# Performance work log

Measured on AMD Instinct MI355X. Metric: run time of the kernel, lower is better.

## Reference

```python
import jax, jax.numpy as jnp
import numpy as np

EMBED = 1024
HEADS = 16
HEAD_DIM = EMBED // HEADS
EPS = 1e-8


def setup_inputs() -> dict:
    key = jax.random.key(0)
    ks = jax.random.split(key, 10)
    s = 1.0 / np.sqrt(EMBED)
    return {
        "hidden_input": jax.random.normal(ks[0], (4, 2048, EMBED), dtype=jnp.float32),
        "Wq": jax.random.uniform(ks[1], (EMBED, EMBED), jnp.float32, -s, s),
        "bq": jax.random.uniform(ks[2], (EMBED,), jnp.float32, -s, s),
        "Wk": jax.random.uniform(ks[3], (EMBED, EMBED), jnp.float32, -s, s),
        "bk": jax.random.uniform(ks[4], (EMBED,), jnp.float32, -s, s),
        "Wv": jax.random.uniform(ks[5], (EMBED, EMBED), jnp.float32, -s, s),
        "bv": jax.random.uniform(ks[6], (EMBED,), jnp.float32, -s, s),
        "Wp": jax.random.uniform(ks[7], (EMBED, EMBED), jnp.float32, -s, s),
        "bp": jax.random.uniform(ks[8], (EMBED,), jnp.float32, -s, s),
        "gamma": jnp.ones((EMBED,), jnp.float32),
        "beta": jnp.zeros((EMBED,), jnp.float32),
    }


def reference(hidden_input, Wq, bq, Wk, bk, Wv, bv, Wp, bp, gamma, beta):
    n, l, e = hidden_input.shape
    h, d = HEADS, HEAD_DIM

    def split_heads(x):  # [n, l, e] -> [n, h, l, d]
        return x.reshape(n, l, h, d).transpose(0, 2, 1, 3)

    q = split_heads(hidden_input @ Wq + bq)
    k = split_heads(hidden_input @ Wk + bk)
    v = split_heads(hidden_input @ Wv + bv)

    scores = jnp.einsum("nhqd,nhkd->nhqk", q, k) / jnp.sqrt(jnp.float32(d))
    attn = jax.nn.softmax(scores, axis=-1)
    ctx = jnp.einsum("nhqk,nhkd->nhqd", attn, v)
    ctx = ctx.transpose(0, 2, 1, 3).reshape(n, l, e)

    out = ctx @ Wp + bp
    x = out + hidden_input
    mu = jnp.mean(x, axis=-1, keepdims=True)
    var = jnp.mean(jnp.square(x - mu), axis=-1, keepdims=True)
    return (x - mu) / jnp.sqrt(var + EPS) * gamma + beta
```

## Files before the change

### kernel.cpp

```cpp
#include <hip/hip_runtime.h>

#define EMBED 1024
#define SEQ   2048
#define BATCH 4
#define HEADS 16

typedef __attribute__((ext_vector_type(8))) short short8;
typedef __attribute__((ext_vector_type(4))) float floatx4;

#define MFMA16(a, b, c) __builtin_amdgcn_mfma_f32_16x16x32_bf16((a), (b), (c), 0, 0, 0)
#define ATT_SCALE (0.125f * 1.44269504088896340736f)

static __device__ __forceinline__ unsigned short f2bf(float f) {
  union { float f; unsigned int u; } v; v.f = f;
  unsigned int u = v.u;
  u += 0x7fffu + ((u >> 16) & 1u);
  return (unsigned short)(u >> 16);
}

static __device__ __forceinline__ void async16(const unsigned short* g, unsigned short* l) {
  __builtin_amdgcn_global_load_lds(
      (const __attribute__((address_space(1))) void*)g,
      (__attribute__((address_space(3))) void*)l, 16, 0, 0);
}

__global__ __launch_bounds__(256) void k_prep(const float* __restrict__ hid,
                                              unsigned short* __restrict__ hidA,
                                              const float* __restrict__ Wq, const float* __restrict__ Wk,
                                              const float* __restrict__ Wv, const float* __restrict__ Wp,
                                              unsigned short* __restrict__ WT) {
  __shared__ unsigned short tile[64][65];
  const int bid = blockIdx.x, tid = threadIdx.x;
  if (bid < 4096) {
    int i = bid * 256 + tid;
    const float4* s = (const float4*)hid;
    float4 a = s[i * 2], b = s[i * 2 + 1];
    uint4 o;
    o.x = (unsigned)f2bf(a.x) | ((unsigned)f2bf(a.y) << 16);
    o.y = (unsigned)f2bf(a.z) | ((unsigned)f2bf(a.w) << 16);
    o.z = (unsigned)f2bf(b.x) | ((unsigned)f2bf(b.y) << 16);
    o.w = (unsigned)f2bf(b.z) | ((unsigned)f2bf(b.w) << 16);
    ((uint4*)hidA)[i] = o;
    return;
  }
  const int idx = bid - 4096;
  const int z = idx >> 8, rem = idx & 255;
  const float* src = (z == 0) ? Wq : (z == 1) ? Wk : (z == 2) ? Wv : Wp;
  unsigned short* dst = WT + (size_t)z * EMBED * EMBED;
  const int k0 = (rem & 15) * 64, n0 = (rem >> 4) * 64;
  for (int i = tid; i < 4096; i += 256) {
    int r = i >> 6, c = i & 63;
    tile[c][r] = f2bf(src[(size_t)(k0 + r) * EMBED + n0 + c]);
  }
  __syncthreads();
  for (int i = tid; i < 4096; i += 256) {
    int r = i >> 6, c = i & 63;
    dst[(size_t)(n0 + r) * EMBED + k0 + c] = tile[r][c];
  }
}

__global__ __launch_bounds__(256) void k_gemm_qkv(const unsigned short* __restrict__ A,
                                                  const unsigned short* __restrict__ BT,
                                                  const float* __restrict__ bq,
                                                  const float* __restrict__ bk,
                                                  const float* __restrict__ bv,
                                                  unsigned short* __restrict__ C) {
  __shared__ unsigned short Als[128 * 64];
  __shared__ unsigned short Bls[128 * 64];
  const int tid = threadIdx.x;
  const int m0 = blockIdx.x * 128, n0 = blockIdx.y * 128;
  const int w = tid >> 6, lane = tid & 63, l16 = lane & 15, quad = lane >> 4;
  const int l7 = l16 & 7;
  const int wrow = (w >> 1) * 64, wcol = (w & 1) * 64;

  floatx4 acc[4][4];
#pragma unroll
  for (int i = 0; i < 4; ++i)
#pragma unroll
    for (int j = 0; j < 4; ++j) acc[i][j] = {0.f, 0.f, 0.f, 0.f};

  const int srow = tid >> 3;
  const int scol = (((tid & 7) ^ (srow & 7)) * 8);
  const unsigned short* Ap = A + (size_t)(m0 + srow) * EMBED + scol;
  const unsigned short* Bp = BT + (size_t)(n0 + srow) * EMBED + scol;

  int ab[2], bb[2];
#pragma unroll
  for (int kc = 0; kc < 2; ++kc) {
    ab[kc] = (wrow + l16) * 64 + (((4 * kc + quad) ^ l7) << 3);
    bb[kc] = (wcol + l16) * 64 + (((4 * kc + quad) ^ l7) << 3);
  }

  for (int kt = 0; kt < 16; ++kt) {
    const int k0 = kt * 64;
#pragma unroll
    for (int i = 0; i < 4; ++i)
      async16(Ap + k0 + (size_t)i * 32 * EMBED, Als + i * 2048 + tid * 8);
#pragma unroll
    for (int i = 0; i < 4; ++i)
      async16(Bp + k0 + (size_t)i * 32 * EMBED, Bls + i * 2048 + tid * 8);
    __syncthreads();
    short8 af[4][2], bf[4][2];
#pragma unroll
    for (int mt = 0; mt < 4; ++mt)
#pragma unroll
      for (int kc = 0; kc < 2; ++kc)
        af[mt][kc] = *(const short8*)(Als + ab[kc] + mt * 1024);
#pragma unroll
    for (int nt = 0; nt < 4; ++nt)
#pragma unroll
      for (int kc = 0; kc < 2; ++kc)
        bf[nt][kc] = *(const short8*)(Bls + bb[kc] + nt * 1024);
#pragma unroll
    for (int kc = 0; kc < 2; ++kc)
#pragma unroll
      for (int mt = 0; mt < 4; ++mt)
#pragma unroll
        for (int nt = 0; nt < 4; ++nt)
          acc[mt][nt] = MFMA16(af[mt][kc], bf[nt][kc], acc[mt][nt]);
    __syncthreads();
  }

  const float* bsel = (n0 < 1024) ? bq : (n0 < 2048 ? bk : bv);
  const float scl = (n0 < 1024) ? ATT_SCALE : 1.0f;
  const int nb = n0 & 1023;
  float bias[4];
#pragma unroll
  for (int nt = 0; nt < 4; ++nt) bias[nt] = bsel[nb + wcol + nt * 16 + l16];
#pragma unroll
  for (int mt = 0; mt < 4; ++mt)
#pragma unroll
    for (int r = 0; r < 4; ++r) {
      int gm = m0 + wrow + mt * 16 + quad * 4 + r;
      size_t base = (size_t)gm * 3072 + n0 + wcol;
#pragma unroll
      for (int nt = 0; nt < 4; ++nt)
        C[base + nt * 16 + l16] = f2bf((acc[mt][nt][r] + bias[nt]) * scl);
    }
}

__global__ __launch_bounds__(256) void k_vt(const unsigned short* __restrict__ QKV,
                                            unsigned short* __restrict__ VT) {
  int lt = blockIdx.x;
  int bh = blockIdx.y;
  int b = bh >> 4, h = bh & 15;
  int l0 = lt * 64;
  __shared__ unsigned short tile[64][65];
  const unsigned short* src = QKV + (size_t)(b * SEQ) * 3072 + 2048 + h * 64;
  unsigned short* dst = VT + (size_t)bh * 64 * SEQ;
  int tid = threadIdx.x;
  for (int i = tid; i < 4096; i += 256) {
    int r = i >> 6, c = i & 63;
    tile[c][r] = src[(size_t)(l0 + r) * 3072 + c];
  }
  __syncthreads();
  for (int i = tid; i < 4096; i += 256) {
    int r = i >> 6, c = i & 63;
    int cp = (c & 15) * 4 + (c >> 4);
    dst[(size_t)r * SEQ + l0 + cp] = tile[r][c];
  }
}

__global__ __launch_bounds__(256, 2) void k_attn(const unsigned short* __restrict__ QKV,
                                                 const unsigned short* __restrict__ VT,
                                                 unsigned short* __restrict__ CTX) {
  const int bh = blockIdx.x, qt = blockIdx.y;
  const int b = bh >> 4, h = bh & 15;
  const int tid = threadIdx.x;
  const int w = tid >> 6, lane = tid & 63, l16 = lane & 15, quad = lane >> 4;

  __shared__ unsigned short Kls[2][64 * 64];
  __shared__ unsigned short Vls[2][64 * 64];
  __shared__ unsigned short Pls[4][64 * 64];

  const unsigned short* Qb = QKV + (size_t)(b * SEQ + qt * 256 + w * 64) * 3072 + h * 64;
  const unsigned short* Kb = QKV + (size_t)(b * SEQ) * 3072 + 1024 + h * 64;
  const unsigned short* Vb = VT + (size_t)bh * 64 * SEQ;
  unsigned short* Pw = Pls[w];

  int pwb[4];
#pragma unroll
  for (int r = 0; r < 4; ++r)
    pwb[r] = (quad * 4 + r) * 64 + ((((l16 >> 1) + quad * 4 + r) & 7) << 3) + ((l16 & 1) << 2);
  int prb[2];
#pragma unroll
  for (int kc = 0; kc < 2; ++kc)
    prb[kc] = l16 * 64 + (((kc * 4 + quad + l16) & 7) << 3);

  short8 qf[4][2];
#pragma unroll
  for (int mt = 0; mt < 4; ++mt)
#pragma unroll
    for (int kc = 0; kc < 2; ++kc)
      qf[mt][kc] = *(const short8*)(Qb + (size_t)(mt * 16 + l16) * 3072 + kc * 32 + quad * 8);

  floatx4 o[4][4];
  float rs[4][4];
#pragma unroll
  for (int mt = 0; mt < 4; ++mt)
#pragma unroll
    for (int nt = 0; nt < 4; ++nt) { o[mt][nt] = {0.f, 0.f, 0.f, 0.f}; rs[mt][nt] = 0.f; }

  const int srow = tid >> 3;
  const int scol = (((tid & 7) ^ (srow & 7)) * 8);

  async16(Kb + (size_t)srow * 3072 + scol, Kls[0] + tid * 8);
  async16(Kb + (size_t)(32 + srow) * 3072 + scol, Kls[0] + 2048 + tid * 8);
  async16(Vb + (size_t)srow * SEQ + scol, Vls[0] + tid * 8);
  async16(Vb + (size_t)(32 + srow) * SEQ + scol, Vls[0] + 2048 + tid * 8);
  __syncthreads();

  int cur = 0;
  for (int kt = 0; kt < 32; ++kt) {
    if (kt < 31) {
      const int kn = (kt + 1) * 64;
      unsigned short* Kd = Kls[cur ^ 1];
      unsigned short* Vd = Vls[cur ^ 1];
      async16(Kb + (size_t)(kn + srow) * 3072 + scol, Kd + tid * 8);
      async16(Kb + (size_t)(kn + 32 + srow) * 3072 + scol, Kd + 2048 + tid * 8);
      async16(Vb + (size_t)srow * SEQ + kn + scol, Vd + tid * 8);
      async16(Vb + (size_t)(32 + srow) * SEQ + kn + scol, Vd + 2048 + tid * 8);
    }
    const unsigned short* Kc = Kls[cur];
    const unsigned short* Vc = Vls[cur];

    short8 kf[4][2];
#pragma unroll
    for (int nt = 0; nt < 4; ++nt)
#pragma unroll
      for (int kc = 0; kc < 2; ++kc) {
        int row = nt * 16 + l16;
        kf[nt][kc] = *(const short8*)(Kc + row * 64 + (((kc * 4 + quad) ^ (row & 7)) * 8));
      }

#pragma unroll
    for (int mt = 0; mt < 4; ++mt) {
      floatx4 s[4];
      __builtin_amdgcn_s_setprio(1);
#pragma unroll
      for (int nt = 0; nt < 4; ++nt) {
        floatx4 z = {0.f, 0.f, 0.f, 0.f};
        z = MFMA16(qf[mt][0], kf[nt][0], z);
        s[nt] = MFMA16(qf[mt][1], kf[nt][1], z);
      }
      __builtin_amdgcn_s_setprio(0);
#pragma unroll
      for (int r = 0; r < 4; ++r) {
        union { float f; unsigned u; } c0, c1, c2, c3;
        c0.f = __builtin_amdgcn_exp2f(s[0][r]);
        c1.f = __builtin_amdgcn_exp2f(s[1][r]);
        c2.f = __builtin_amdgcn_exp2f(s[2][r]);
        c3.f = __builtin_amdgcn_exp2f(s[3][r]);
        rs[mt][r] += (c0.f + c1.f) + (c2.f + c3.f);
        uint2 pk;
        pk.x = __builtin_amdgcn_perm(c1.u, c0.u, 0x07060302);
        pk.y = __builtin_amdgcn_perm(c3.u, c2.u, 0x07060302);
        *(uint2*)(Pw + pwb[r] + mt * 1024) = pk;
      }
    }

    __asm__ volatile("s_waitcnt lgkmcnt(0)" ::: "memory");

    short8 vf[4][2];
#pragma unroll
    for (int nt = 0; nt < 4; ++nt)
#pragma unroll
      for (int kc = 0; kc < 2; ++kc) {
        int row = nt * 16 + l16;
        vf[nt][kc] = *(const short8*)(Vc + row * 64 + (((kc * 4 + quad) ^ (row & 7)) * 8));
      }
    __builtin_amdgcn_s_setprio(1);
#pragma unroll
    for (int kc = 0; kc < 2; ++kc)
#pragma unroll
      for (int mt = 0; mt < 4; ++mt) {
        short8 pf = *(const short8*)(Pw + prb[kc] + mt * 1024);
#pragma unroll
        for (int nt = 0; nt < 4; ++nt)
          o[mt][nt] = MFMA16(pf, vf[nt][kc], o[mt][nt]);
      }
    __builtin_amdgcn_s_setprio(0);

    __syncthreads();
    cur ^= 1;
  }

#pragma unroll
  for (int mt = 0; mt < 4; ++mt)
#pragma unroll
    for (int r = 0; r < 4; ++r) {
      float v = rs[mt][r];
#pragma unroll
      for (int off = 1; off < 16; off <<= 1) v += __shfl_xor(v, off);
      rs[mt][r] = 1.f / v;
    }

#pragma unroll
  for (int mt = 0; mt < 4; ++mt)
#pragma unroll
    for (int r = 0; r < 4; ++r) {
      int gq = b * SEQ + qt * 256 + w * 64 + mt * 16 + quad * 4 + r;
      float inv = rs[mt][r];
      size_t base = (size_t)gq * EMBED + h * 64;
#pragma unroll
      for (int nt = 0; nt < 4; ++nt)
        CTX[base + nt * 16 + l16] = f2bf(o[mt][nt][r] * inv);
    }
}

__global__ __launch_bounds__(256) void k_gemm_proj(const unsigned short* __restrict__ A,
                                                   const unsigned short* __restrict__ BT,
                                                   const float* __restrict__ bp,
                                                   const float* __restrict__ hid,
                                                   float* __restrict__ X) {
  __shared__ unsigned short Als[128 * 64];
  __shared__ unsigned short Bls[128 * 64];
  const int tid = threadIdx.x;
  const int m0 = blockIdx.x * 128, n0 = blockIdx.y * 128;
  const int w = tid >> 6, lane = tid & 63, l16 = lane & 15, quad = lane >> 4;
  const int l7 = l16 & 7;
  const int wrow = (w >> 1) * 64, wcol = (w & 1) * 64;

  floatx4 acc[4][4];
#pragma unroll
  for (int i = 0; i < 4; ++i)
#pragma unroll
    for (int j = 0; j < 4; ++j) acc[i][j] = {0.f, 0.f, 0.f, 0.f};

  const int srow = tid >> 3;
  const int scol = (((tid & 7) ^ (srow & 7)) * 8);
  const unsigned short* Ap = A + (size_t)(m0 + srow) * EMBED + scol;
  const unsigned short* Bp = BT + (size_t)(n0 + srow) * EMBED + scol;

  int ab[2], bb[2];
#pragma unroll
  for (int kc = 0; kc < 2; ++kc) {
    ab[kc] = (wrow + l16) * 64 + (((4 * kc + quad) ^ l7) << 3);
    bb[kc] = (wcol + l16) * 64 + (((4 * kc + quad) ^ l7) << 3);
  }

  for (int kt = 0; kt < 16; ++kt) {
    const int k0 = kt * 64;
#pragma unroll
    for (int i = 0; i < 4; ++i)
      async16(Ap + k0 + (size_t)i * 32 * EMBED, Als + i * 2048 + tid * 8);
#pragma unroll
    for (int i = 0; i < 4; ++i)
      async16(Bp + k0 + (size_t)i * 32 * EMBED, Bls + i * 2048 + tid * 8);
    __syncthreads();
    short8 af[4][2], bf[4][2];
#pragma unroll
    for (int mt = 0; mt < 4; ++mt)
#pragma unroll
      for (int kc = 0; kc < 2; ++kc)
        af[mt][kc] = *(const short8*)(Als + ab[kc] + mt * 1024);
#pragma unroll
    for (int nt = 0; nt < 4; ++nt)
#pragma unroll
      for (int kc = 0; kc < 2; ++kc)
        bf[nt][kc] = *(const short8*)(Bls + bb[kc] + nt * 1024);
#pragma unroll
    for (int kc = 0; kc < 2; ++kc)
#pragma unroll
      for (int mt = 0; mt < 4; ++mt)
#pragma unroll
        for (int nt = 0; nt < 4; ++nt)
          acc[mt][nt] = MFMA16(af[mt][kc], bf[nt][kc], acc[mt][nt]);
    __syncthreads();
  }

  float bias[4];
#pragma unroll
  for (int nt = 0; nt < 4; ++nt) bias[nt] = bp[n0 + wcol + nt * 16 + l16];
#pragma unroll
  for (int mt = 0; mt < 4; ++mt)
#pragma unroll
    for (int r = 0; r < 4; ++r) {
      int gm = m0 + wrow + mt * 16 + quad * 4 + r;
      size_t base = (size_t)gm * EMBED + n0 + wcol;
#pragma unroll
      for (int nt = 0; nt < 4; ++nt) {
        size_t idx = base + nt * 16 + l16;
        X[idx] = acc[mt][nt][r] + bias[nt] + hid[idx];
      }
    }
}

__global__ __launch_bounds__(256) void k_ln(float* __restrict__ x,
                                            const float* __restrict__ gamma,
                                            const float* __restrict__ beta) {
  int row = blockIdx.x, tid = threadIdx.x;
  float4* rp = (float4*)(x + (size_t)row * EMBED);
  float4 v = rp[tid];
  float s = v.x + v.y + v.z + v.w;
  float q = v.x * v.x + v.y * v.y + v.z * v.z + v.w * v.w;
#pragma unroll
  for (int off = 1; off < 64; off <<= 1) {
    s += __shfl_xor(s, off);
    q += __shfl_xor(q, off);
  }
  __shared__ float ss[4], sq[4];
  int w = tid >> 6;
  if ((tid & 63) == 0) { ss[w] = s; sq[w] = q; }
  __syncthreads();
  s = ss[0] + ss[1] + ss[2] + ss[3];
  q = sq[0] + sq[1] + sq[2] + sq[3];
  float mean = s * (1.f / 1024.f);
  float var = q * (1.f / 1024.f) - mean * mean;
  float rstd = rsqrtf(var + 1e-8f);
  float4 g = ((const float4*)gamma)[tid];
  float4 be = ((const float4*)beta)[tid];
  v.x = (v.x - mean) * rstd * g.x + be.x;
  v.y = (v.y - mean) * rstd * g.y + be.y;
  v.z = (v.z - mean) * rstd * g.z + be.z;
  v.w = (v.w - mean) * rstd * g.w + be.w;
  rp[tid] = v;
}

extern "C" void kernel_launch(void* const* d_in, const int* in_sizes, int n_in,
                              void* d_out, int out_size, void* d_ws, size_t ws_size,
                              hipStream_t stream) {
  const float* hid   = (const float*)d_in[0];
  const float* Wq    = (const float*)d_in[1];
  const float* bq    = (const float*)d_in[2];
  const float* Wk    = (const float*)d_in[3];
  const float* bk    = (const float*)d_in[4];
  const float* Wv    = (const float*)d_in[5];
  const float* bv    = (const float*)d_in[6];
  const float* Wp    = (const float*)d_in[7];
  const float* bp    = (const float*)d_in[8];
  const float* gamma = (const float*)d_in[9];
  const float* beta  = (const float*)d_in[10];
  float* out = (float*)d_out;

  char* ws = (char*)d_ws;
  unsigned short* hidA = (unsigned short*)ws;
  unsigned short* WT   = (unsigned short*)(ws + (size_t)(16 << 20));
  unsigned short* QKV  = (unsigned short*)(ws + (size_t)(24 << 20));
  unsigned short* VT   = (unsigned short*)(ws + (size_t)(72 << 20));
  unsigned short* CTX  = (unsigned short*)(ws + (size_t)(88 << 20));

  k_prep<<<5120, 256, 0, stream>>>(hid, hidA, Wq, Wk, Wv, Wp, WT);
  k_gemm_qkv<<<dim3(64, 24), 256, 0, stream>>>(hidA, WT, bq, bk, bv, QKV);
  k_vt<<<dim3(32, 64), 256, 0, stream>>>(QKV, VT);
  k_attn<<<dim3(64, 8), 256, 0, stream>>>(QKV, VT, CTX);
  k_gemm_proj<<<dim3(64, 8), 256, 0, stream>>>(CTX, WT + (size_t)3 * EMBED * EMBED, bp, hid, out);
  k_ln<<<8192, 256, 0, stream>>>(out, gamma, beta);
}
```

Measured before the change: 287.6 us.

## Switch attention to 32x32 MFMA with register-resident P via permlane swap

```diff
diff --git a/kernel.cpp b/kernel.cpp
--- a/kernel.cpp
+++ b/kernel.cpp
@@ -7,8 +7,10 @@
 
 typedef __attribute__((ext_vector_type(8))) short short8;
 typedef __attribute__((ext_vector_type(4))) float floatx4;
+typedef __attribute__((ext_vector_type(16))) float floatx16;
 
 #define MFMA16(a, b, c) __builtin_amdgcn_mfma_f32_16x16x32_bf16((a), (b), (c), 0, 0, 0)
+#define MFMA32(a, b, c) __builtin_amdgcn_mfma_f32_32x32x16_bf16((a), (b), (c), 0, 0, 0)
 #define ATT_SCALE (0.125f * 1.44269504088896340736f)
 
 static __device__ __forceinline__ unsigned short f2bf(float f) {
@@ -16,6 +18,12 @@
   unsigned int u = v.u;
   u += 0x7fffu + ((u >> 16) & 1u);
   return (unsigned short)(u >> 16);
+}
+
+static __device__ __forceinline__ unsigned cvtpk(float lo, float hi) {
+  unsigned r;
+  asm("v_cvt_pk_bf16_f32 %0, %1, %2" : "=v"(r) : "v"(lo), "v"(hi));
+  return r;
 }
 
 static __device__ __forceinline__ void async16(const unsigned short* g, unsigned short* l) {
@@ -156,8 +164,7 @@
   __syncthreads();
   for (int i = tid; i < 4096; i += 256) {
     int r = i >> 6, c = i & 63;
-    int cp = (c & 15) * 4 + (c >> 4);
-    dst[(size_t)r * SEQ + l0 + cp] = tile[r][c];
+    dst[(size_t)r * SEQ + l0 + c] = tile[r][c];
   }
 }
 
@@ -167,39 +174,32 @@
   const int bh = blockIdx.x, qt = blockIdx.y;
   const int b = bh >> 4, h = bh & 15;
   const int tid = threadIdx.x;
-  const int w = tid >> 6, lane = tid & 63, l16 = lane & 15, quad = lane >> 4;
+  const int w = tid >> 6, lane = tid & 63;
+  const int l32 = lane & 31, hi = lane >> 5;
 
   __shared__ unsigned short Kls[2][64 * 64];
   __shared__ unsigned short Vls[2][64 * 64];
-  __shared__ unsigned short Pls[4][64 * 64];
+  __shared__ float rsls[4][64];
 
   const unsigned short* Qb = QKV + (size_t)(b * SEQ + qt * 256 + w * 64) * 3072 + h * 64;
   const unsigned short* Kb = QKV + (size_t)(b * SEQ) * 3072 + 1024 + h * 64;
   const unsigned short* Vb = VT + (size_t)bh * 64 * SEQ;
-  unsigned short* Pw = Pls[w];
-
-  int pwb[4];
-#pragma unroll
-  for (int r = 0; r < 4; ++r)
-    pwb[r] = (quad * 4 + r) * 64 + ((((l16 >> 1) + quad * 4 + r) & 7) << 3) + ((l16 & 1) << 2);
-  int prb[2];
-#pragma unroll
-  for (int kc = 0; kc < 2; ++kc)
-    prb[kc] = l16 * 64 + (((kc * 4 + quad + l16) & 7) << 3);
-
-  short8 qf[4][2];
-#pragma unroll
-  for (int mt = 0; mt < 4; ++mt)
-#pragma unroll
-    for (int kc = 0; kc < 2; ++kc)
-      qf[mt][kc] = *(const short8*)(Qb + (size_t)(mt * 16 + l16) * 3072 + kc * 32 + quad * 8);
-
-  floatx4 o[4][4];
-  float rs[4][4];
-#pragma unroll
-  for (int mt = 0; mt < 4; ++mt)
-#pragma unroll
-    for (int nt = 0; nt < 4; ++nt) { o[mt][nt] = {0.f, 0.f, 0.f, 0.f}; rs[mt][nt] = 0.f; }
+
+  short8 qf[2][4];
+#pragma unroll
+  for (int qg = 0; qg < 2; ++qg)
+#pragma unroll
+    for (int ds = 0; ds < 4; ++ds)
+      qf[qg][ds] = *(const short8*)(Qb + (size_t)(qg * 32 + l32) * 3072 + ds * 16 + hi * 8);
+
+  floatx16 o[2][2];
+  float rs[2] = {0.f, 0.f};
+#pragma unroll
+  for (int qg = 0; qg < 2; ++qg)
+#pragma unroll
+    for (int dg = 0; dg < 2; ++dg)
+#pragma unroll
+      for (int c = 0; c < 16; ++c) o[qg][dg][c] = 0.f;
 
   const int srow = tid >> 3;
   const int scol = (((tid & 7) ^ (srow & 7)) * 8);
@@ -224,87 +224,79 @@
     const unsigned short* Kc = Kls[cur];
     const unsigned short* Vc = Vls[cur];
 
-    short8 kf[4][2];
-#pragma unroll
-    for (int nt = 0; nt < 4; ++nt)
-#pragma unroll
-      for (int kc = 0; kc < 2; ++kc) {
-        int row = nt * 16 + l16;
-        kf[nt][kc] = *(const short8*)(Kc + row * 64 + (((kc * 4 + quad) ^ (row & 7)) * 8));
+    short8 pa[2][4];
+#pragma unroll
+    for (int kvg = 0; kvg < 2; ++kvg) {
+      short8 kf[4];
+#pragma unroll
+      for (int ds = 0; ds < 4; ++ds) {
+        const int row = kvg * 32 + l32;
+        kf[ds] = *(const short8*)(Kc + row * 64 + (((ds * 2 + hi) ^ (row & 7)) << 3));
       }
-
-#pragma unroll
-    for (int mt = 0; mt < 4; ++mt) {
-      floatx4 s[4];
-      __builtin_amdgcn_s_setprio(1);
-#pragma unroll
-      for (int nt = 0; nt < 4; ++nt) {
-        floatx4 z = {0.f, 0.f, 0.f, 0.f};
-        z = MFMA16(qf[mt][0], kf[nt][0], z);
-        s[nt] = MFMA16(qf[mt][1], kf[nt][1], z);
+#pragma unroll
+      for (int qg = 0; qg < 2; ++qg) {
+        floatx16 s;
+#pragma unroll
+        for (int c = 0; c < 16; ++c) s[c] = 0.f;
+#pragma unroll
+        for (int ds = 0; ds < 4; ++ds) s = MFMA32(kf[ds], qf[qg][ds], s);
+        float p[16];
+#pragma unroll
+        for (int c = 0; c < 16; ++c) p[c] = __builtin_amdgcn_exp2f(s[c]);
+        rs[qg] += (((p[0] + p[1]) + (p[2] + p[3])) + ((p[4] + p[5]) + (p[6] + p[7])))
+                + (((p[8] + p[9]) + (p[10] + p[11])) + ((p[12] + p[13]) + (p[14] + p[15])));
+#pragma unroll
+        for (int half = 0; half < 2; ++half) {
+          unsigned w0 = cvtpk(p[half * 8 + 0], p[half * 8 + 1]);
+          unsigned w1 = cvtpk(p[half * 8 + 2], p[half * 8 + 3]);
+          unsigned w2 = cvtpk(p[half * 8 + 4], p[half * 8 + 5]);
+          unsigned w3 = cvtpk(p[half * 8 + 6], p[half * 8 + 7]);
+          asm("v_permlane32_swap_b32 %0, %1" : "+v"(w0), "+v"(w2));
+          asm("v_permlane32_swap_b32 %0, %1" : "+v"(w1), "+v"(w3));
+          union { unsigned u[4]; short8 s8; } pk;
+          pk.u[0] = w0; pk.u[1] = w1; pk.u[2] = w2; pk.u[3] = w3;
+          pa[qg][kvg * 2 + half] = pk.s8;
+        }
       }
-      __builtin_amdgcn_s_setprio(0);
-#pragma unroll
-      for (int r = 0; r < 4; ++r) {
-        union { float f; unsigned u; } c0, c1, c2, c3;
-        c0.f = __builtin_amdgcn_exp2f(s[0][r]);
-        c1.f = __builtin_amdgcn_exp2f(s[1][r]);
-        c2.f = __builtin_amdgcn_exp2f(s[2][r]);
-        c3.f = __builtin_amdgcn_exp2f(s[3][r]);
-        rs[mt][r] += (c0.f + c1.f) + (c2.f + c3.f);
-        uint2 pk;
-        pk.x = __builtin_amdgcn_perm(c1.u, c0.u, 0x07060302);
-        pk.y = __builtin_amdgcn_perm(c3.u, c2.u, 0x07060302);
-        *(uint2*)(Pw + pwb[r] + mt * 1024) = pk;
+    }
+
+#pragma unroll
+    for (int dg = 0; dg < 2; ++dg) {
+      short8 vf[4];
+#pragma unroll
+      for (int ks = 0; ks < 4; ++ks) {
+        const int row = dg * 32 + l32;
+        vf[ks] = *(const short8*)(Vc + row * 64 + (((ks * 2 + hi) ^ (row & 7)) << 3));
       }
-    }
-
-    __asm__ volatile("s_waitcnt lgkmcnt(0)" ::: "memory");
-
-    short8 vf[4][2];
-#pragma unroll
-    for (int nt = 0; nt < 4; ++nt)
-#pragma unroll
-      for (int kc = 0; kc < 2; ++kc) {
-        int row = nt * 16 + l16;
-        vf[nt][kc] = *(const short8*)(Vc + row * 64 + (((kc * 4 + quad) ^ (row & 7)) * 8));
-      }
-    __builtin_amdgcn_s_setprio(1);
-#pragma unroll
-    for (int kc = 0; kc < 2; ++kc)
-#pragma unroll
-      for (int mt = 0; mt < 4; ++mt) {
-        short8 pf = *(const short8*)(Pw + prb[kc] + mt * 1024);
-#pragma unroll
-        for (int nt = 0; nt < 4; ++nt)
-          o[mt][nt] = MFMA16(pf, vf[nt][kc], o[mt][nt]);
-      }
-    __builtin_amdgcn_s_setprio(0);
+#pragma unroll
+      for (int qg = 0; qg < 2; ++qg)
+#pragma unroll
+        for (int ks = 0; ks < 4; ++ks)
+          o[qg][dg] = MFMA32(pa[qg][ks], vf[ks], o[qg][dg]);
+    }
 
     __syncthreads();
     cur ^= 1;
   }
 
-#pragma unroll
-  for (int mt = 0; mt < 4; ++mt)
-#pragma unroll
-    for (int r = 0; r < 4; ++r) {
-      float v = rs[mt][r];
-#pragma unroll
-      for (int off = 1; off < 16; off <<= 1) v += __shfl_xor(v, off);
-      rs[mt][r] = 1.f / v;
-    }
-
-#pragma unroll
-  for (int mt = 0; mt < 4; ++mt)
-#pragma unroll
-    for (int r = 0; r < 4; ++r) {
-      int gq = b * SEQ + qt * 256 + w * 64 + mt * 16 + quad * 4 + r;
-      float inv = rs[mt][r];
-      size_t base = (size_t)gq * EMBED + h * 64;
-#pragma unroll
-      for (int nt = 0; nt < 4; ++nt)
-        CTX[base + nt * 16 + l16] = f2bf(o[mt][nt][r] * inv);
+  rs[0] += __shfl_xor(rs[0], 32);
+  rs[1] += __shfl_xor(rs[1], 32);
+  if (lane < 32) {
+    rsls[w][l32] = rs[0];
+    rsls[w][32 + l32] = rs[1];
+  }
+
+#pragma unroll
+  for (int qg = 0; qg < 2; ++qg)
+#pragma unroll
+    for (int j = 0; j < 16; ++j) {
+      const int rl = (j & 3) + 8 * (j >> 2) + 4 * hi;
+      const float inv = 1.f / rsls[w][qg * 32 + rl];
+      const int gq = b * SEQ + qt * 256 + w * 64 + qg * 32 + rl;
+      const size_t base = (size_t)gq * EMBED + h * 64;
+#pragma unroll
+      for (int dg = 0; dg < 2; ++dg)
+        CTX[base + dg * 32 + l32] = f2bf(o[qg][dg][j] * inv);
     }
 }
 
```

New measurement: 279.3 us. 2.9% less time.
